# Kernel optimization log

Measured on AMD Instinct MI355X. Metric: run time of the kernel, lower is better.

Reference implementation:

```python
import jax, jax.numpy as jnp
import numpy as np

T, C, NH, NL, NP = 5, 192, 4, 5, 4
DH = C // NH

def leaky(x):
    return jnp.where(x >= 0, x, 0.1 * x)

def conv2d(x, w, b, padding=1, dilation=1):
    out = jax.lax.conv_general_dilated(
        x, w, window_strides=(1, 1),
        padding=[(padding, padding), (padding, padding)],
        rhs_dilation=(dilation, dilation),
        dimension_numbers=('NCHW', 'OIHW', 'NCHW'))
    return out + b[None, :, None, None]

def grid_sample_border(img, gx, gy):
    # align_corners=True, padding_mode='border'; gx/gy normalized [-1,1], shape (B,H,W)
    B, Cc, H, W = img.shape
    x = jnp.clip((gx + 1.0) * 0.5 * (W - 1), 0.0, W - 1)
    y = jnp.clip((gy + 1.0) * 0.5 * (H - 1), 0.0, H - 1)
    x0 = jnp.floor(x); y0 = jnp.floor(y)
    wx = (x - x0).reshape(B, 1, -1); wy = (y - y0).reshape(B, 1, -1)
    flat = img.reshape(B, Cc, H * W)
    def g(yi, xi):
        xi = jnp.clip(xi, 0, W - 1).astype(jnp.int32)
        yi = jnp.clip(yi, 0, H - 1).astype(jnp.int32)
        return jnp.take_along_axis(flat, (yi * W + xi).reshape(B, 1, -1), axis=2)
    out = (g(y0, x0) * (1 - wx) * (1 - wy) + g(y0, x0 + 1) * wx * (1 - wy)
         + g(y0 + 1, x0) * (1 - wx) * wy + g(y0 + 1, x0 + 1) * wx * wy)
    return out.reshape(B, Cc, H, W)

def warp(x, flo):
    B, _, H, W = x.shape
    xx = jnp.arange(W, dtype=jnp.float32)[None, :] * jnp.ones((H, 1), jnp.float32)
    yy = jnp.arange(H, dtype=jnp.float32)[:, None] * jnp.ones((1, W), jnp.float32)
    gx = 2.0 * (xx[None] + flo[:, 0]) / max(W - 1, 1) - 1.0
    gy = 2.0 * (yy[None] + flo[:, 1]) / max(H - 1, 1) - 1.0
    return grid_sample_border(x, gx, gy)

def deform_sample(v_img, loc):
    # v_img (N,D,H,W); loc (N,Q,P,2) in [0,1]; bilinear, zeros padding, align_corners=False
    N, D, H, W = v_img.shape
    Q, P = loc.shape[1], loc.shape[2]
    x = loc[..., 0] * W - 0.5
    y = loc[..., 1] * H - 0.5
    x0 = jnp.floor(x); y0 = jnp.floor(y)
    wx = (x - x0).reshape(N, 1, -1); wy = (y - y0).reshape(N, 1, -1)
    flat = v_img.reshape(N, D, H * W)
    def g(yi, xi):
        valid = ((xi >= 0) & (xi <= W - 1) & (yi >= 0) & (yi <= H - 1)).astype(v_img.dtype)
        xi_c = jnp.clip(xi, 0, W - 1).astype(jnp.int32)
        yi_c = jnp.clip(yi, 0, H - 1).astype(jnp.int32)
        return jnp.take_along_axis(flat, (yi_c * W + xi_c).reshape(N, 1, -1), axis=2) * valid.reshape(N, 1, -1)
    out = (g(y0, x0) * (1 - wx) * (1 - wy) + g(y0, x0 + 1) * wx * (1 - wy)
         + g(y0 + 1, x0) * (1 - wx) * wy + g(y0 + 1, x0 + 1) * wx * wy)
    return out.reshape(N, D, Q, P)

def _forward(frame, srcframe, flow_forward, flow_backward,
             w_qk, b_qk, w_v, b_v, w_vproj, b_vproj, w_off, b_off,
             w_attn, b_attn, w_out, b_out, w_ff, b_ff,
             w_ffn1, b_ffn1, w_ffn2, b_ffn2):
    b, t, c, h, w = frame.shape
    ff01, ff12 = flow_forward[:, 0], flow_forward[:, 1]
    fb32, fb43 = flow_backward[:, 2], flow_backward[:, 3]
    ff02 = ff01 + warp(ff12, ff01)
    fb42 = fb43 + warp(fb32, fb43)
    warp02 = warp(frame[:, 0], ff02)
    warp12 = warp(frame[:, 1], ff12)
    warp32 = warp(frame[:, 3], fb32)
    warp42 = warp(frame[:, 4], fb42)
    qk_in = jnp.concatenate([warp02, warp12, frame[:, 2], warp32, warp42,
                             flow_forward.reshape(b, -1, h, w),
                             flow_backward.reshape(b, -1, h, w)], axis=1)
    queries = leaky(conv2d(qk_in, w_qk, b_qk)).reshape(b, t, c, h, w)
    value = leaky(conv2d(frame.reshape(b, t * c, h, w), w_v, b_v)).reshape(b, t, c, h, w)

    Lq = t * h * w
    q_tok = queries.transpose(0, 1, 3, 4, 2).reshape(b, Lq, c)
    v_tok = value.transpose(0, 1, 3, 4, 2).reshape(b, Lq, c)
    v_proj = (v_tok @ w_vproj.T + b_vproj).reshape(b, t, h * w, NH, DH)

    offs = (q_tok @ w_off.T + b_off).reshape(b, Lq, NH, NL, NP, 2)
    aw = (q_tok @ w_attn.T + b_attn).reshape(b, Lq, NH, NL * NP)
    aw = jax.nn.softmax(aw, axis=-1).reshape(b, Lq, NH, NL, NP)

    # reference points (all valid ratios are ones): ((x+0.5)/W, (y+0.5)/H)
    rx = (jnp.arange(w, dtype=frame.dtype) + 0.5) / w
    ry = (jnp.arange(h, dtype=frame.dtype) + 0.5) / h
    ref = jnp.stack(jnp.meshgrid(rx, ry, indexing='xy'), axis=-1).reshape(h * w, 2)
    ref = jnp.tile(ref, (t, 1))  # (Lq, 2)

    norm = jnp.array([w, h], dtype=frame.dtype)
    # flow-guided per-level displacement toward the center frame (level 2)
    zero = jnp.zeros_like(ff12)
    flows = jnp.stack([ff02, ff12, zero, fb32, fb42], axis=1)  # (b,NL,2,h,w)
    flow_norm = (flows / norm[None, None, :, None, None]).transpose(0, 1, 3, 4, 2).reshape(b, NL, h * w, 2)
    flow_norm = jnp.tile(flow_norm.transpose(0, 2, 1, 3), (1, t, 1, 1))  # (b,Lq,NL,2)

    loc = (ref[None, :, None, None, None, :]
           + offs / norm[None, None, None, None, None, :]
           + flow_norm[:, :, None, :, None, :])  # (b,Lq,NH,NL,NP,2)

    acc = jnp.zeros((b * NH, DH, Lq), dtype=frame.dtype)
    for l in range(NL):
        v_l = v_proj[:, l].transpose(0, 2, 3, 1).reshape(b * NH, DH, h, w)
        loc_l = loc[:, :, :, l].transpose(0, 2, 1, 3, 4).reshape(b * NH, Lq, NP, 2)
        samp = deform_sample(v_l, loc_l)  # (b*NH, DH, Lq, NP)
        w_l = aw[:, :, :, l].transpose(0, 2, 1, 3).reshape(b * NH, 1, Lq, NP)
        acc = acc + (samp * w_l).sum(-1)
    attn = acc.reshape(b, NH, DH, Lq).transpose(0, 3, 1, 2).reshape(b, Lq, c)
    attn = attn @ w_out.T + b_out

    out = attn.reshape(b, t, h, w, c).transpose(0, 1, 4, 2, 3).reshape(b * t, c, h, w)
    out = conv2d(out, w_ff, b_ff)
    out = out.reshape(b, t, c, h, w) + frame
    seq_in = jnp.concatenate([out.reshape(b * t, c, h, w), srcframe.reshape(b * t, c, h, w)], axis=1)
    ffn = conv2d(seq_in, w_ffn1, b_ffn1, padding=2, dilation=2)
    ffn = conv2d(leaky(ffn), w_ffn2, b_ffn2)
    out = out.reshape(b * t, c, h, w) + ffn
    return out.reshape(b, t, c, h, w)

def setup_inputs():
    key = jax.random.key(0)
    ks = jax.random.split(key, 16)
    B, H, W = 2, 64, 64
    s = 0.02
    d = {}
    d['frame'] = jax.random.normal(ks[0], (B, T, C, H, W), jnp.float32)
    d['srcframe'] = jax.random.normal(ks[1], (B, T, C, H, W), jnp.float32)
    d['flow_forward'] = jax.random.normal(ks[2], (B, 4, 2, H, W), jnp.float32)
    d['flow_backward'] = jax.random.normal(ks[3], (B, 4, 2, H, W), jnp.float32)
    cin_qk = T * C + 4 * (T - 1)
    d['w_qk'] = jax.random.normal(ks[4], (T * C, cin_qk, 3, 3), jnp.float32) * s
    d['b_qk'] = jnp.zeros((T * C,), jnp.float32)
    d['w_v'] = jax.random.normal(ks[5], (T * C, T * C, 3, 3), jnp.float32) * s
    d['b_v'] = jnp.zeros((T * C,), jnp.float32)
    d['w_vproj'] = jax.random.normal(ks[6], (C, C), jnp.float32) * s
    d['b_vproj'] = jnp.zeros((C,), jnp.float32)
    d['w_off'] = jax.random.normal(ks[7], (NH * NL * NP * 2, C), jnp.float32) * s
    d['b_off'] = jax.random.normal(ks[8], (NH * NL * NP * 2,), jnp.float32)
    d['w_attn'] = jax.random.normal(ks[9], (NH * NL * NP, C), jnp.float32) * s
    d['b_attn'] = jnp.zeros((NH * NL * NP,), jnp.float32)
    d['w_out'] = jax.random.normal(ks[10], (C, C), jnp.float32) * s
    d['b_out'] = jnp.zeros((C,), jnp.float32)
    d['w_ff'] = jax.random.normal(ks[11], (C, C, 3, 3), jnp.float32) * s
    d['b_ff'] = jnp.zeros((C,), jnp.float32)
    d['w_ffn1'] = jax.random.normal(ks[12], (C, 2 * C, 3, 3), jnp.float32) * s
    d['b_ffn1'] = jnp.zeros((C,), jnp.float32)
    d['w_ffn2'] = jax.random.normal(ks[13], (C, C, 3, 3), jnp.float32) * s
    d['b_ffn2'] = jnp.zeros((C,), jnp.float32)
    return d

def reference(frame, srcframe, flow_forward, flow_backward, w_qk, b_qk, w_v, b_v, w_vproj, b_vproj, w_off, b_off, w_attn, b_attn, w_out, b_out, w_ff, b_ff, w_ffn1, b_ffn1, w_ffn2, b_ffn2):
    out = _forward(frame, srcframe, flow_forward, flow_backward, w_qk, b_qk, w_v, b_v, w_vproj, b_vproj, w_off, b_off, w_attn, b_attn, w_out, b_out, w_ff, b_ff, w_ffn1, b_ffn1, w_ffn2, b_ffn2)
    return (out, srcframe)
```

## Files before the change

### kernel.cpp

```cpp
#include <hip/hip_runtime.h>


#define HWPX 4096
#define PPXN 4624
#define LQ   20480

typedef __attribute__((ext_vector_type(8))) short  short8;
typedef __attribute__((ext_vector_type(4))) short  short4v;
typedef __attribute__((ext_vector_type(4))) float  f32x4;
typedef __attribute__((ext_vector_type(4))) float  float4v;

__device__ __forceinline__ unsigned short f2bf(float f) {
    unsigned u = __float_as_uint(f);
    unsigned r = (u + 0x7FFF + ((u >> 16) & 1)) >> 16;
    return (unsigned short)r;
}
__device__ __forceinline__ float bf2f(unsigned short s) {
    return __uint_as_float(((unsigned)s) << 16);
}

__device__ __forceinline__ void gl_lds16(const unsigned short* g, unsigned short* l) {
    __builtin_amdgcn_global_load_lds(
        (const __attribute__((address_space(1))) unsigned int*)g,
        (__attribute__((address_space(3))) unsigned int*)l, 16, 0, 0);
}

__device__ __forceinline__ float bsample(const float* __restrict__ p, float sx, float sy) {
    sx = fminf(fmaxf(sx, 0.f), 63.f);
    sy = fminf(fmaxf(sy, 0.f), 63.f);
    float x0 = floorf(sx), y0 = floorf(sy);
    int ix0 = (int)x0, iy0 = (int)y0;
    int ix1 = ix0 < 63 ? ix0 + 1 : 63;
    int iy1 = iy0 < 63 ? iy0 + 1 : 63;
    float wx = sx - x0, wy = sy - y0;
    float v00 = p[iy0*64+ix0], v01 = p[iy0*64+ix1];
    float v10 = p[iy1*64+ix0], v11 = p[iy1*64+ix1];
    return (v00*(1.f-wx) + v01*wx)*(1.f-wy) + (v10*(1.f-wx) + v11*wx)*wy;
}

__device__ void dev_flow(int i, const float* __restrict__ ff,
                         const float* __restrict__ fb, float* __restrict__ flows) {
    int b = i >> 12, pix = i & 4095;
    int x = pix & 63, y = pix >> 6;
    const float* ff01 = ff + (size_t)(b*4+0)*2*HWPX;
    const float* ff12 = ff + (size_t)(b*4+1)*2*HWPX;
    const float* fb32 = fb + (size_t)(b*4+2)*2*HWPX;
    const float* fb43 = fb + (size_t)(b*4+3)*2*HWPX;
    float* F = flows + (size_t)b*5*2*HWPX;
    float ax = ff01[pix], ay = ff01[HWPX+pix];
    float sx = bsample(ff12,      (float)x+ax, (float)y+ay);
    float sy = bsample(ff12+HWPX, (float)x+ax, (float)y+ay);
    F[0*2*HWPX + pix]        = ax + sx;
    F[0*2*HWPX + HWPX + pix] = ay + sy;
    F[1*2*HWPX + pix]        = ff12[pix];
    F[1*2*HWPX + HWPX + pix] = ff12[HWPX+pix];
    F[2*2*HWPX + pix]        = 0.f;
    F[2*2*HWPX + HWPX + pix] = 0.f;
    F[3*2*HWPX + pix]        = fb32[pix];
    F[3*2*HWPX + HWPX + pix] = fb32[HWPX+pix];
    float bx = fb43[pix], by = fb43[HWPX+pix];
    float tx = bsample(fb32,      (float)x+bx, (float)y+by);
    float ty = bsample(fb32+HWPX, (float)x+bx, (float)y+by);
    F[4*2*HWPX + pix]        = bx + tx;
    F[4*2*HWPX + HWPX + pix] = by + ty;
}

__device__ void dev_wT(const float* __restrict__ w, unsigned short* __restrict__ wT,
                       int CI, int NKB, int cotile, int kblk, int tid) {
    unsigned short* dst = wT + ((size_t)(cotile*NKB + kblk))*18432;
    #pragma unroll
    for (int it = 0; it < 9; ++it) {
        int idx = it*256 + tid;
        int tap = idx >> 8, sub = idx & 255;
        int cg = sub >> 6, co = sub & 63;
        int cog = cotile*64 + co;
        int ci0 = kblk*32 + cg*8;
        short8 v;
        #pragma unroll
        for (int j = 0; j < 8; ++j) {
            int ci = ci0 + j;
            v[j] = (ci < CI) ? (short)f2bf(w[((size_t)cog*CI + ci)*9 + tap]) : (short)0;
        }
        *(short8*)(dst + (size_t)idx*8) = v;
    }
}

__device__ void dev_wg(const float* __restrict__ w1, const float* __restrict__ w2,
                       unsigned short* __restrict__ wg, int co_split, int CO,
                       int cotile, int tid) {
    unsigned short* dst = wg + (size_t)cotile*12288;
    #pragma unroll
    for (int it = 0; it < 6; ++it) {
        int idx = it*256 + tid;
        int kblk = idx >> 8, sub = idx & 255;
        int cg = sub >> 6, co = sub & 63;
        int cog = cotile*64 + co;
        int ci0 = kblk*32 + cg*8;
        short8 v = {};
        if (cog < CO) {
            const float* row = (cog < co_split) ? w1 + (size_t)cog*192
                                                : w2 + (size_t)(cog - co_split)*192;
            #pragma unroll
            for (int j = 0; j < 8; ++j) v[j] = (short)f2bf(row[ci0 + j]);
        }
        *(short8*)(dst + (size_t)idx*8) = v;
    }
}

__device__ void dev_pad(const float* __restrict__ in, unsigned short* __restrict__ outb,
                        int CI, int PITCH, int COFF, int img, int ppx_t, int cq, int tid) {
    int ppx = ppx_t*64 + (tid & 63);
    if (ppx >= PPXN) return;
    int c8 = (cq*4 + (tid >> 6))*8;
    unsigned short* dst = outb + ((size_t)img*PPXN + ppx)*PITCH;
    int py = ppx/68, pxc = ppx - py*68;
    if (py < 2 || py >= 66 || pxc < 2 || pxc >= 66) {
        short8 z = {};
        *(short8*)(dst + c8) = z;
        if (COFF) *(short8*)(dst + COFF + c8) = z;
        return;
    }
    int pix = ((py-2)<<6) + (pxc-2);
    short8 o;
    #pragma unroll
    for (int j = 0; j < 8; ++j)
        o[j] = (short)f2bf(in[((size_t)img*CI + c8 + j)*HWPX + pix]);
    *(short8*)(dst + COFF + c8) = o;
}

__global__ __launch_bounds__(256) void k_wprep(
    const float* __restrict__ flow_f, const float* __restrict__ flow_b,
    float* __restrict__ flows,
    const float* __restrict__ w_qk, unsigned short* __restrict__ wT_qk,
    const float* __restrict__ w_v,  unsigned short* __restrict__ wT_v,
    const float* __restrict__ w_ff, unsigned short* __restrict__ wT_ff,
    const float* __restrict__ w_f1, unsigned short* __restrict__ wT_f1,
    const float* __restrict__ w_f2, unsigned short* __restrict__ wT_f2,
    const float* __restrict__ w_vp, const float* __restrict__ w_off,
    const float* __restrict__ w_at, const float* __restrict__ w_out,
    unsigned short* __restrict__ wg_vp, unsigned short* __restrict__ wg_oa,
    unsigned short* __restrict__ wg_out,
    const float* __restrict__ srcframe, float* __restrict__ out2)
{
    int bid = blockIdx.x, tid = threadIdx.x;
    if (bid < 32) {
        dev_flow(bid*256 + tid, flow_f, flow_b, flows);
    } else if (bid < 497) {
        int p = bid - 32;   dev_wT(w_qk, wT_qk, 976, 31, p/31, p%31, tid);
    } else if (bid < 947) {
        int p = bid - 497;  dev_wT(w_v,  wT_v,  960, 30, p/30, p%30, tid);
    } else if (bid < 965) {
        int p = bid - 947;  dev_wT(w_ff, wT_ff, 192, 6,  p/6,  p%6,  tid);
    } else if (bid < 1001) {
        int p = bid - 965;  dev_wT(w_f1, wT_f1, 384, 12, p/12, p%12, tid);
    } else if (bid < 1019) {
        int p = bid - 1001; dev_wT(w_f2, wT_f2, 192, 6,  p/6,  p%6,  tid);
    } else if (bid < 1029) {
        int g = bid - 1019;
        if (g < 3)      dev_wg(w_vp,  nullptr, wg_vp, 192, 192, g,   tid);
        else if (g < 7) dev_wg(w_off, w_at,    wg_oa, 160, 240, g-3, tid);
        else            dev_wg(w_out, nullptr, wg_out, 192, 192, g-7, tid);
    } else {
        int c = bid - 1029;
        const float4v* s4 = (const float4v*)srcframe;
        float4v* d4 = (float4v*)out2;
        #pragma unroll
        for (int it = 0; it < 8; ++it) {
            int idx = it*245760 + c*256 + tid;
            d4[idx] = s4[idx];
        }
    }
}

__global__ void k_qkin(const unsigned short* __restrict__ Pv,
                       const float* __restrict__ ff, const float* __restrict__ fb,
                       const float* __restrict__ flows,
                       unsigned short* __restrict__ Pqk)
{
    int ppx = blockIdx.x*64 + threadIdx.x;
    if (ppx >= PPXN) return;
    int b = blockIdx.z;
    int c8 = (blockIdx.y*4 + threadIdx.y)*8;
    unsigned short* dst = Pqk + ((size_t)b*PPXN + ppx)*992 + c8;
    int py = ppx/68, pxc = ppx - py*68;
    short8 o = {};
    if (py >= 2 && py < 66 && pxc >= 2 && pxc < 66 && c8 < 976) {
        int y = py-2, x = pxc-2, pix = (y<<6)+x;
        if (c8 >= 960) {
            #pragma unroll
            for (int j = 0; j < 8; ++j) {
                int k = c8 - 960 + j;
                float v = (k < 8) ? ff[((size_t)b*8 + k)*HWPX + pix]
                                  : fb[((size_t)b*8 + k - 8)*HWPX + pix];
                o[j] = (short)f2bf(v);
            }
        } else {
            const unsigned short* Pvb = Pv + (size_t)b*PPXN*960;
            int slot = c8/192;
            if (slot == 2) {
                o = *(const short8*)(Pvb + (size_t)ppx*960 + c8);
            } else {
                const float* F = flows + ((size_t)(b*5 + slot)*2)*HWPX;
                float sx = fminf(fmaxf((float)x + F[pix], 0.f), 63.f);
                float sy = fminf(fmaxf((float)y + F[HWPX + pix], 0.f), 63.f);
                float x0 = floorf(sx), y0 = floorf(sy);
                int ix0 = (int)x0, iy0 = (int)y0;
                int ix1 = ix0 < 63 ? ix0+1 : 63, iy1 = iy0 < 63 ? iy0+1 : 63;
                float wx = sx - x0, wy = sy - y0;
                float w00 = (1.f-wx)*(1.f-wy), w01 = wx*(1.f-wy);
                float w10 = (1.f-wx)*wy,       w11 = wx*wy;
                short8 v00 = *(const short8*)(Pvb + ((size_t)((iy0+2)*68 + ix0+2))*960 + c8);
                short8 v01 = *(const short8*)(Pvb + ((size_t)((iy0+2)*68 + ix1+2))*960 + c8);
                short8 v10 = *(const short8*)(Pvb + ((size_t)((iy1+2)*68 + ix0+2))*960 + c8);
                short8 v11 = *(const short8*)(Pvb + ((size_t)((iy1+2)*68 + ix1+2))*960 + c8);
                #pragma unroll
                for (int j = 0; j < 8; ++j) {
                    float v = bf2f((unsigned short)v00[j])*w00 + bf2f((unsigned short)v01[j])*w01
                            + bf2f((unsigned short)v10[j])*w10 + bf2f((unsigned short)v11[j])*w11;
                    o[j] = (short)f2bf(v);
                }
            }
        }
    }
    *(short8*)dst = o;
}

__global__ void t_pad(const float* __restrict__ in, unsigned short* __restrict__ outb,
                      int CI, int PITCH, int COFF)
{
    int ppx = blockIdx.x*64 + threadIdx.x;
    if (ppx >= PPXN) return;
    int img = blockIdx.z;
    int c8 = (blockIdx.y*4 + threadIdx.y)*8;
    unsigned short* dst = outb + ((size_t)img*PPXN + ppx)*PITCH;
    int py = ppx/68, pxc = ppx - py*68;
    if (py < 2 || py >= 66 || pxc < 2 || pxc >= 66) {
        short8 z = {};
        *(short8*)(dst + c8) = z;
        if (COFF) *(short8*)(dst + COFF + c8) = z;
        return;
    }
    int pix = ((py-2)<<6) + (pxc-2);
    short8 o;
    #pragma unroll
    for (int j = 0; j < 8; ++j)
        o[j] = (short)f2bf(in[((size_t)img*CI + c8 + j)*HWPX + pix]);
    *(short8*)(dst + COFF + c8) = o;
}

template<int ROWS, int DIL, int OUTK, bool LEAKY, int RESK>
__global__ __launch_bounds__(256, 2) void k_conv(
    const unsigned short* __restrict__ P0, const unsigned short* __restrict__ P1,
    int CIP0, int CIP1, int NKB0, int NKB1,
    const unsigned short* __restrict__ wT0, const unsigned short* __restrict__ wT1,
    const float* __restrict__ bias0, const float* __restrict__ bias1,
    const float* __restrict__ resF, const unsigned short* __restrict__ resB, int resPitch,
    float* __restrict__ outF,
    unsigned short* __restrict__ outB0, unsigned short* __restrict__ outB1,
    int outPitch, int outCoff, int njobs)
{
    constexpr int RR     = ROWS*4 + 2*DIL;
    constexpr int XP     = 64 + 2*DIL;
    constexpr int PLANE  = RR*XP*16;
    constexpr int NCH    = RR*XP*4;
    constexpr int NXS    = (NCH + 255)/256;
    constexpr int TILEPX = ROWS*4*64;
    constexpr int SMEM_K = 4*PLANE + 36864;
    constexpr int SMEM_E = (OUTK <= 1) ? TILEPX*72*2 : 0;
    constexpr int SMEMSZ = SMEM_K > SMEM_E ? SMEM_K : SMEM_E;
    __shared__ __align__(16) unsigned char smem[SMEMSZ];
    unsigned char*  s_x = smem;
    unsigned short* s_w = (unsigned short*)(smem + 4*PLANE);

    int tid = threadIdx.x & 255;
    int gx = gridDim.x, gy = gridDim.y, gz = gridDim.z;
    int lin = blockIdx.x + gx*(blockIdx.y + gy*blockIdx.z);
    int tot = gx*gy*gz;
    if ((tot & 7) == 0) { int q = tot >> 3; lin = (lin & 7)*q + (lin >> 3); }
    int cotile = lin % gx; int rem = lin / gx;
    int ytile = rem % gy;  int z = rem / gy;

    int sel = (njobs == 2) ? (z >> 1) : 0;
    int img = (njobs == 2) ? (z & 1)  : z;
    const unsigned short* P  = sel ? P1  : P0;
    const unsigned short* wT = sel ? wT1 : wT0;
    const float* bias        = sel ? bias1 : bias0;
    unsigned short* outB     = sel ? outB1 : outB0;
    int CIP = sel ? CIP1 : CIP0;
    int NKB = sel ? NKB1 : NKB0;

    int y0 = ytile * (ROWS*4);
    const unsigned short* Pi = P + (size_t)img*PPXN*CIP;
    int w = tid >> 6, lane = tid & 63, lm = lane & 15, cig = lane >> 4;

    auto stage_x = [&](int kb) {
        int k0 = kb*32;
        #pragma unroll
        for (int it = 0; it < NXS; ++it) {
            int li = it*256 + tid;
            if (li < NCH) {
                int p = li / (RR*XP), rm = li - p*(RR*XP);
                int r = rm / XP, c = rm - r*XP;
                gl_lds16(Pi + ((size_t)((y0 + 2 - DIL + r)*68 + c + 2 - DIL))*CIP + k0 + p*8,
                         (unsigned short*)(s_x + li*16));
            }
        }
    };
    auto stage_w = [&](int kb) {
        const unsigned short* ws = wT + ((size_t)(cotile*NKB + kb))*18432;
        #pragma unroll
        for (int it = 0; it < 9; ++it)
            gl_lds16(ws + (size_t)(it*256+tid)*8, &s_w[(it*256+tid)*8]);
    };

    stage_x(0); stage_w(0);
    __syncthreads();

    f32x4 acc[4][ROWS*4] = {};
    for (int kb = 0; kb < NKB; ++kb) {
        __builtin_amdgcn_s_setprio(1);
        #pragma unroll
        for (int t = 0; t < 9; ++t) {
            int ky = t/3, kx = t - ky*3;
            short8 A[4];
            #pragma unroll
            for (int mb = 0; mb < 4; ++mb)
                A[mb] = *(const short8*)&s_w[((t*4 + cig)*64 + mb*16 + lm)*8];
            #pragma unroll
            for (int s = 0; s < ROWS; ++s) {
                short8 Bf[4];
                #pragma unroll
                for (int nc = 0; nc < 4; ++nc)
                    Bf[nc] = *(const short8*)&s_x[cig*PLANE +
                               ((w*ROWS + s + ky*DIL)*XP + nc*16 + lm + kx*DIL)*16];
                #pragma unroll
                for (int mb = 0; mb < 4; ++mb)
                    #pragma unroll
                    for (int nc = 0; nc < 4; ++nc)
                        acc[mb][s*4+nc] = __builtin_amdgcn_mfma_f32_16x16x32_bf16(
                            A[mb], Bf[nc], acc[mb][s*4+nc], 0, 0, 0);
            }
        }
        __builtin_amdgcn_s_setprio(0);
        __syncthreads();
        if (kb + 1 < NKB) { stage_x(kb+1); stage_w(kb+1); }
        __syncthreads();
    }

    if (OUTK == 0 || OUTK == 1) {
        unsigned short* epi = (unsigned short*)smem;
        #pragma unroll
        for (int mb = 0; mb < 4; ++mb) {
            int cob = cotile*64 + mb*16 + cig*4;
            int col = mb*16 + cig*4;
            #pragma unroll
            for (int s = 0; s < ROWS; ++s) {
                int lr = w*ROWS + s;
                #pragma unroll
                for (int nc = 0; nc < 4; ++nc) {
                    int x = nc*16 + lm;
                    int px_l = lr*64 + x;
                    int gpx = y0*64 + px_l;
                    short4v sv;
                    #pragma unroll
                    for (int r = 0; r < 4; ++r) {
                        float v = acc[mb][s*4+nc][r] + bias[cob + r];
                        if (LEAKY) v = v >= 0.f ? v : 0.1f*v;
                        if (RESK == 1) v += resF[((size_t)img*192 + cob + r)*HWPX + gpx];
                        sv[r] = (short)f2bf(v);
                    }
                    *(short4v*)&epi[px_l*72 + col] = sv;
                }
            }
        }
        __syncthreads();
        constexpr int NCPY = TILEPX/32;
        int slot = (OUTK == 0) ? (cotile*64)/192 : 0;
        int ccb  = (OUTK == 0) ? (cotile*64)%192 : (cotile*64 + outCoff);
        #pragma unroll
        for (int it2 = 0; it2 < NCPY; ++it2) {
            int li = it2*256 + tid;
            int px_l = li >> 3, sub = li & 7;
            short8 v = *(const short8*)&epi[px_l*72 + sub*8];
            int gpx = y0*64 + px_l;
            if (OUTK == 0) {
                *(short8*)(outB + ((size_t)(img*5 + slot)*HWPX + gpx)*192 + ccb + sub*8) = v;
            } else {
                int ppx = ((gpx>>6)+2)*68 + (gpx&63) + 2;
                *(short8*)(outB0 + ((size_t)img*PPXN + ppx)*outPitch + ccb + sub*8) = v;
            }
        }
    } else {
        #pragma unroll
        for (int mb = 0; mb < 4; ++mb) {
            int cob = cotile*64 + mb*16 + cig*4;
            #pragma unroll
            for (int s = 0; s < ROWS; ++s) {
                int y = y0 + w*ROWS + s;
                #pragma unroll
                for (int nc = 0; nc < 4; ++nc) {
                    int x = nc*16 + lm;
                    int px = (y<<6) + x;
                    int ppx = (y+2)*68 + x + 2;
                    short4v rv;
                    if (RESK == 2)
                        rv = *(const short4v*)(resB + ((size_t)img*PPXN + ppx)*resPitch + cob);
                    #pragma unroll
                    for (int r = 0; r < 4; ++r) {
                        float v = acc[mb][s*4+nc][r] + bias[cob + r];
                        if (LEAKY) v = v >= 0.f ? v : 0.1f*v;
                        if (RESK == 1) v += resF[((size_t)img*192 + cob + r)*HWPX + px];
                        if (RESK == 2) v += bf2f((unsigned short)rv[r]);
                        outF[((size_t)img*192 + cob + r)*HWPX + px] = v;
                    }
                }
            }
        }
    }
}

#define GEMM_CORE(Xi, WG_, cotile_)                                              \
    _Pragma("unroll")                                                            \
    for (int it = 0; it < 6; ++it)                                               \
        gl_lds16(WG_ + (size_t)(cotile_)*12288 + (it*256+tid)*8,                 \
                 &s_w[(it*256+tid)*8]);                                          \
    short8 xr[4];                                                                \
    _Pragma("unroll")                                                            \
    for (int it = 0; it < 4; ++it)                                               \
        xr[it] = *(const short8*)(Xi + (size_t)(px0 + tid)*192 + it*8);          \
    _Pragma("unroll")                                                            \
    for (int it = 0; it < 4; ++it)                                               \
        *(short8*)&s_x[0][it*4096 + tid*16] = xr[it];                            \
    __syncthreads();                                                             \
    int w = tid >> 6, lane = tid & 63, lm = lane & 15, cig = lane >> 4;          \
    f32x4 acc[4][4] = {};                                                        \
    int xb = 0;                                                                  \
    for (int kb = 0; kb < 6; ++kb) {                                             \
        bool pf = (kb < 5);                                                      \
        if (pf) {                                                                \
            int k0 = (kb+1)*32;                                                  \
            _Pragma("unroll")                                                    \
            for (int it = 0; it < 4; ++it)                                       \
                xr[it] = *(const short8*)(Xi + (size_t)(px0 + tid)*192 + k0 + it*8); \
        }                                                                        \
        short8 A[4], Bf[4];                                                      \
        _Pragma("unroll")                                                        \
        for (int nb = 0; nb < 4; ++nb)                                           \
            Bf[nb] = *(const short8*)&s_x[xb][cig*4096 + (w*64 + nb*16 + lm)*16];\
        _Pragma("unroll")                                                        \
        for (int mb = 0; mb < 4; ++mb)                                           \
            A[mb] = *(const short8*)&s_w[((kb*4 + cig)*64 + mb*16 + lm)*8];      \
        _Pragma("unroll")                                                        \
        for (int mb = 0; mb < 4; ++mb)                                           \
            _Pragma("unroll")                                                    \
            for (int nb = 0; nb < 4; ++nb)                                       \
                acc[mb][nb] = __builtin_amdgcn_mfma_f32_16x16x32_bf16(           \
                    A[mb], Bf[nb], acc[mb][nb], 0, 0, 0);                        \
        if (pf) {                                                                \
            _Pragma("unroll")                                                    \
            for (int it = 0; it < 4; ++it)                                       \
                *(short8*)&s_x[xb^1][it*4096 + tid*16] = xr[it];                 \
        }                                                                        \
        __syncthreads();                                                         \
        xb ^= 1;                                                                 \
    }

__global__ __launch_bounds__(256) void k_gemmA(
    const unsigned short* __restrict__ Xv, const unsigned short* __restrict__ WGv,
    const float* __restrict__ bvp, unsigned short* __restrict__ vp,
    const unsigned short* __restrict__ Xq, const unsigned short* __restrict__ WGq,
    const float* __restrict__ boff, const float* __restrict__ batt,
    float* __restrict__ offs, float* __restrict__ aw,
    unsigned short* __restrict__ P_ff, unsigned short* __restrict__ P_mid)
{
    __shared__ unsigned char  s_x[2][4*4096];
    __shared__ unsigned short s_w[12288];
    int tid = threadIdx.x & 255;
    int id = blockIdx.x;
    if (id < 480) {
        int cotile = id % 3, pxt = (id/3) % 16, img = id/48;
        int px0 = pxt*256;
        const unsigned short* Xi = Xv + (size_t)img*HWPX*192;
        GEMM_CORE(Xi, WGv, cotile)
        #pragma unroll
        for (int mb = 0; mb < 4; ++mb) {
            int cob = cotile*64 + mb*16 + cig*4;
            int h = cob/48, d = cob - h*48;
            #pragma unroll
            for (int nb = 0; nb < 4; ++nb) {
                int px = px0 + w*64 + nb*16 + lm;
                short4v s;
                #pragma unroll
                for (int r = 0; r < 4; ++r)
                    s[r] = (short)f2bf(acc[mb][nb][r] + bvp[cob + r]);
                *(short4v*)(vp + (((size_t)img*4 + h)*HWPX + px)*48 + d) = s;
            }
        }
    } else if (id < 1120) {
        int i2 = id - 480;
        int cotile = i2 % 4, pxt = (i2/4) % 16, img = i2/64;
        int px0 = pxt*256;
        const unsigned short* Xi = Xq + (size_t)img*HWPX*192;
        GEMM_CORE(Xi, WGq, cotile)
        int b = img/5, t = img - b*5;
        #pragma unroll
        for (int mb = 0; mb < 4; ++mb) {
            int cob = cotile*64 + mb*16 + cig*4;
            if (cob >= 240) continue;
            #pragma unroll
            for (int nb = 0; nb < 4; ++nb) {
                int px = px0 + w*64 + nb*16 + lm;
                #pragma unroll
                for (int r = 0; r < 4; ++r) {
                    int co = cob + r;
                    float bv = (co < 160) ? boff[co] : batt[co-160];
                    float v = acc[mb][nb][r] + bv;
                    if (co < 160) offs[((size_t)b*160 + co)*LQ + t*HWPX + px] = v;
                    else          aw[((size_t)b*80 + co-160)*LQ + t*HWPX + px] = v;
                }
            }
        }
    } else {
        int u = (id - 1120)*256 + tid;
        int c8i = u % 24; int r1 = u / 24;
        int b = r1 % 528; int r2 = r1 / 528;
        int img = r2 % 10; int buf = r2 / 10;
        int ppx;
        if (b < 136) ppx = b;
        else if (b < 272) ppx = 4488 + (b - 136);
        else { int b2 = b - 272; int row = 2 + (b2 >> 2); int cs = b2 & 3;
               ppx = row*68 + ((cs < 2) ? cs : cs + 64); }
        unsigned short* bp2 = buf ? P_mid : P_ff;
        short8 z = {};
        *(short8*)(bp2 + ((size_t)img*PPXN + ppx)*192 + c8i*8) = z;
    }
}

__global__ __launch_bounds__(256) void k_tailB(
    const unsigned short* __restrict__ X, const unsigned short* __restrict__ WG,
    const float* __restrict__ b1, unsigned short* __restrict__ P_ff,
    const float* __restrict__ srcframe, unsigned short* __restrict__ P_ffn1)
{
    __shared__ unsigned char  s_x[2][4*4096];
    __shared__ unsigned short s_w[12288];
    int tid = threadIdx.x & 255;
    int id = blockIdx.x;
    if (id < 480) {
        int cotile = id % 3, pxt = (id/3) % 16, img = id/48;
        int px0 = pxt*256;
        const unsigned short* Xi = X + (size_t)img*HWPX*192;
        GEMM_CORE(Xi, WG, cotile)
        #pragma unroll
        for (int mb = 0; mb < 4; ++mb) {
            int cob = cotile*64 + mb*16 + cig*4;
            #pragma unroll
            for (int nb = 0; nb < 4; ++nb) {
                int px = px0 + w*64 + nb*16 + lm;
                int ppx = ((px>>6)+2)*68 + (px&63) + 2;
                short4v s;
                #pragma unroll
                for (int r = 0; r < 4; ++r)
                    s[r] = (short)f2bf(acc[mb][nb][r] + b1[cob + r]);
                *(short4v*)(P_ff + ((size_t)img*PPXN + ppx)*192 + cob) = s;
            }
        }
    } else {
        int p = id - 480;
        int img = p / 438, rem = p - img*438;
        int ppx_t = rem % 73, cq = rem / 73;
        dev_pad(srcframe, P_ffn1, 192, 384, 192, img, ppx_t, cq, tid);
    }
}

__device__ __forceinline__ void addtap24(float* acc, const unsigned short* __restrict__ src, float w) {
    const short8* s8 = (const short8*)src;
    #pragma unroll
    for (int u = 0; u < 3; ++u) {
        short8 v = s8[u];
        #pragma unroll
        for (int j = 0; j < 8; ++j)
            acc[u*8+j] += w * bf2f((unsigned short)v[j]);
    }
}

__global__ __launch_bounds__(256) void k_sample(
    const unsigned short* __restrict__ vp, const float* __restrict__ offs,
    const float* __restrict__ aw, const float* __restrict__ flows,
    unsigned short* __restrict__ accout)
{
    int blk = blockIdx.x;
    int b = blk / 640, sub = blk - b*640;
    int tid = threadIdx.x;
    int lq = sub*32 + (tid >> 3);
    int h = (tid >> 1) & 3, q = tid & 1;
    int pix = lq & 4095;
    int x = pix & 63, y = pix >> 6;
    const float* offp = offs + ((size_t)b*160 + h*40)*LQ + lq;
    const float* awp  = aw   + ((size_t)b*80  + h*20)*LQ + lq;
    float e[20];
    float m = -1e30f;
    #pragma unroll
    for (int j = 0; j < 20; ++j) { e[j] = awp[(size_t)j*LQ]; m = fmaxf(m, e[j]); }
    float ssum = 0.f;
    #pragma unroll
    for (int j = 0; j < 20; ++j) { e[j] = __expf(e[j]-m); ssum += e[j]; }
    float inv = 1.f/ssum;

    float acc[24];
    #pragma unroll
    for (int d = 0; d < 24; ++d) acc[d] = 0.f;

    for (int l = 0; l < 5; ++l) {
        float fx = flows[((size_t)(b*5+l)*2+0)*HWPX + pix];
        float fy = flows[((size_t)(b*5+l)*2+1)*HWPX + pix];
        const unsigned short* vpl = vp + (((size_t)(b*5+l)*4 + h)*HWPX)*48 + q*24;
        #pragma unroll
        for (int p = 0; p < 4; ++p) {
            int o = l*4 + p;
            float ox = offp[(size_t)(2*o)*LQ];
            float oy = offp[(size_t)(2*o+1)*LQ];
            float wv = e[o]*inv;
            float sx = (float)x + ox + fx;
            float sy = (float)y + oy + fy;
            float x0f = floorf(sx), y0f = floorf(sy);
            float wx = sx - x0f, wy = sy - y0f;
            int ix0 = (int)x0f, iy0 = (int)y0f;
            float w00 = wv*(1.f-wx)*(1.f-wy), w01 = wv*wx*(1.f-wy);
            float w10 = wv*(1.f-wx)*wy,       w11 = wv*wx*wy;
            bool vx0 = (ix0 >= 0)  && (ix0 <= 63);
            bool vx1 = (ix0 >= -1) && (ix0 <= 62);
            bool vy0 = (iy0 >= 0)  && (iy0 <= 63);
            bool vy1 = (iy0 >= -1) && (iy0 <= 62);
            if (vy0 && vx0) addtap24(acc, vpl + (size_t)(iy0*64 + ix0)*48,       w00);
            if (vy0 && vx1) addtap24(acc, vpl + (size_t)(iy0*64 + ix0 + 1)*48,   w01);
            if (vy1 && vx0) addtap24(acc, vpl + (size_t)((iy0+1)*64 + ix0)*48,   w10);
            if (vy1 && vx1) addtap24(acc, vpl + (size_t)((iy0+1)*64 + ix0+1)*48, w11);
        }
    }
    unsigned short* dst = accout + ((size_t)b*LQ + lq)*192 + h*48 + q*24;
    #pragma unroll
    for (int u = 0; u < 3; ++u) {
        short8 s;
        #pragma unroll
        for (int j = 0; j < 8; ++j) s[j] = (short)f2bf(acc[u*8+j]);
        *(short8*)(dst + u*8) = s;
    }
}


extern "C" void kernel_launch(void* const* d_in, const int* in_sizes, int n_in,
                              void* d_out, int out_size, void* d_ws, size_t ws_size,
                              hipStream_t stream) {
    (void)in_sizes; (void)n_in; (void)out_size; (void)ws_size;
    const float* frame    = (const float*)d_in[0];
    const float* srcframe = (const float*)d_in[1];
    const float* flow_f   = (const float*)d_in[2];
    const float* flow_b   = (const float*)d_in[3];
    const float* w_qk  = (const float*)d_in[4];  const float* b_qk  = (const float*)d_in[5];
    const float* w_v   = (const float*)d_in[6];  const float* b_v   = (const float*)d_in[7];
    const float* w_vp  = (const float*)d_in[8];  const float* b_vp  = (const float*)d_in[9];
    const float* w_off = (const float*)d_in[10]; const float* b_off = (const float*)d_in[11];
    const float* w_at  = (const float*)d_in[12]; const float* b_at  = (const float*)d_in[13];
    const float* w_out = (const float*)d_in[14]; const float* b_out = (const float*)d_in[15];
    const float* w_ff  = (const float*)d_in[16]; const float* b_ff  = (const float*)d_in[17];
    const float* w_f1  = (const float*)d_in[18]; const float* b_f1  = (const float*)d_in[19];
    const float* w_f2  = (const float*)d_in[20]; const float* b_f2  = (const float*)d_in[21];
    float* out = (float*)d_out;
    char* W = (char*)d_ws;

    float*          flows  = (float*)(W + 0);
    unsigned short* wT_qk  = (unsigned short*)(W + 327680);
    unsigned short* wT_v   = (unsigned short*)(W + 17469440);
    unsigned short* P_qk   = (unsigned short*)(W + 34058240);
    unsigned short* P_ff   = P_qk;
    unsigned short* P_v    = (unsigned short*)(W + 52406272);
    unsigned short* P_mid  = P_v;
    unsigned short* Q_tok  = (unsigned short*)(W + 70162432);
    unsigned short* acc_tok= Q_tok;
    unsigned short* V_tok  = (unsigned short*)(W + 85891072);
    unsigned short* P_ffn1 = V_tok;
    unsigned short* vp     = (unsigned short*)(W + 101619712);
    float*          offs   = (float*)(W + 121403392);
    float*          aw     = (float*)(W + 147617792);
    unsigned short* wT_ff  = (unsigned short*)(W + 160724992);
    unsigned short* wT_f1  = (unsigned short*)(W + 161388544);
    unsigned short* wT_f2  = (unsigned short*)(W + 162715648);
    unsigned short* wg_vp  = (unsigned short*)(W + 163379200);
    unsigned short* wg_oa  = (unsigned short*)(W + 163452928);
    unsigned short* wg_out = (unsigned short*)(W + 163551232);

    dim3 bp(64, 4);

    k_wprep<<<1989, 256, 0, stream>>>(
        flow_f, flow_b, flows,
        w_qk, wT_qk, w_v, wT_v, w_ff, wT_ff, w_f1, wT_f1, w_f2, wT_f2,
        w_vp, w_off, w_at, w_out, wg_vp, wg_oa, wg_out,
        srcframe, out + (size_t)2*5*192*HWPX);
    t_pad<<<dim3(73,30,2), bp, 0, stream>>>(frame, P_v, 960, 960, 0);
    k_qkin<<<dim3(73,31,2), bp, 0, stream>>>(P_v, flow_f, flow_b, flows, P_qk);
    k_conv<2,1,0,true,0><<<dim3(15,8,4), 256, 0, stream>>>(
        P_qk, P_v, 992, 960, 31, 30, wT_qk, wT_v, b_qk, b_v,
        nullptr, nullptr, 0, nullptr, Q_tok, V_tok, 0, 0, 2);
    k_gemmA<<<2110, 256, 0, stream>>>(
        V_tok, wg_vp, b_vp, vp, Q_tok, wg_oa, b_off, b_at, offs, aw, P_ff, P_mid);
    k_sample<<<1280, 256, 0, stream>>>(vp, offs, aw, flows, acc_tok);
    k_tailB<<<4860, 256, 0, stream>>>(acc_tok, wg_out, b_out, P_ff,
                                      srcframe, P_ffn1);
    k_conv<1,1,1,false,1><<<dim3(3,16,10), 256, 0, stream>>>(
        P_ff, nullptr, 192, 0, 6, 0, wT_ff, nullptr, b_ff, nullptr,
        frame, nullptr, 0, nullptr, P_ffn1, nullptr, 384, 0, 1);
    k_conv<1,2,1,true,0><<<dim3(3,16,10), 256, 0, stream>>>(
        P_ffn1, nullptr, 384, 0, 12, 0, wT_f1, nullptr, b_f1, nullptr,
        nullptr, nullptr, 0, nullptr, P_mid, nullptr, 192, 0, 1);
    k_conv<1,1,2,false,2><<<dim3(3,16,10), 256, 0, stream>>>(
        P_mid, nullptr, 192, 0, 6, 0, wT_f2, nullptr, b_f2, nullptr,
        nullptr, P_ffn1, 384, out, nullptr, nullptr, 0, 0, 1);
}
```

Baseline: 807.8 us.

## Split deformable sampling points across thread pairs and fold padding into prep kernel

k_sample now splits the 20 sampling points of each query/head across two threads, each handling 10 points. The two partial accumulators are combined with a shuffle-xor reduction and only one thread writes, so twice as many blocks run with fewer serial gathers per thread. Separately, the frame padding/bf16 conversion kernel is merged into the k_wprep launch as extra blocks, removing one kernel launch. The cost is extra shuffles and more blocks in the sampling kernel. Merging also ties the pad work to the prep kernel's block scheduling.

```diff
diff --git a/kernel.cpp b/kernel.cpp
--- a/kernel.cpp
+++ b/kernel.cpp
@@ -140,7 +140,8 @@
     const float* __restrict__ w_at, const float* __restrict__ w_out,
     unsigned short* __restrict__ wg_vp, unsigned short* __restrict__ wg_oa,
     unsigned short* __restrict__ wg_out,
-    const float* __restrict__ srcframe, float* __restrict__ out2)
+    const float* __restrict__ srcframe, float* __restrict__ out2,
+    const float* __restrict__ frame, unsigned short* __restrict__ P_v)
 {
     int bid = blockIdx.x, tid = threadIdx.x;
     if (bid < 32) {
@@ -160,7 +161,7 @@
         if (g < 3)      dev_wg(w_vp,  nullptr, wg_vp, 192, 192, g,   tid);
         else if (g < 7) dev_wg(w_off, w_at,    wg_oa, 160, 240, g-3, tid);
         else            dev_wg(w_out, nullptr, wg_out, 192, 192, g-7, tid);
-    } else {
+    } else if (bid < 1989) {
         int c = bid - 1029;
         const float4v* s4 = (const float4v*)srcframe;
         float4v* d4 = (float4v*)out2;
@@ -169,6 +170,11 @@
             int idx = it*245760 + c*256 + tid;
             d4[idx] = s4[idx];
         }
+    } else {
+        int p = bid - 1989;
+        int img = p / 2190, rem = p - img*2190;
+        int ppx_t = rem % 73, cq = rem / 73;
+        dev_pad(frame, P_v, 960, 960, 0, img, ppx_t, cq, tid);
     }
 }
 
@@ -223,29 +229,6 @@
         }
     }
     *(short8*)dst = o;
-}
-
-__global__ void t_pad(const float* __restrict__ in, unsigned short* __restrict__ outb,
-                      int CI, int PITCH, int COFF)
-{
-    int ppx = blockIdx.x*64 + threadIdx.x;
-    if (ppx >= PPXN) return;
-    int img = blockIdx.z;
-    int c8 = (blockIdx.y*4 + threadIdx.y)*8;
-    unsigned short* dst = outb + ((size_t)img*PPXN + ppx)*PITCH;
-    int py = ppx/68, pxc = ppx - py*68;
-    if (py < 2 || py >= 66 || pxc < 2 || pxc >= 66) {
-        short8 z = {};
-        *(short8*)(dst + c8) = z;
-        if (COFF) *(short8*)(dst + COFF + c8) = z;
-        return;
-    }
-    int pix = ((py-2)<<6) + (pxc-2);
-    short8 o;
-    #pragma unroll
-    for (int j = 0; j < 8; ++j)
-        o[j] = (short)f2bf(in[((size_t)img*CI + c8 + j)*HWPX + pix]);
-    *(short8*)(dst + COFF + c8) = o;
 }
 
 template<int ROWS, int DIL, int OUTK, bool LEAKY, int RESK>
@@ -589,10 +572,12 @@
     unsigned short* __restrict__ accout)
 {
     int blk = blockIdx.x;
-    int b = blk / 640, sub = blk - b*640;
+    int b = blk / 1280, sub = blk - b*1280;
     int tid = threadIdx.x;
-    int lq = sub*32 + (tid >> 3);
-    int h = (tid >> 1) & 3, q = tid & 1;
+    int lq = sub*16 + (tid >> 4);
+    int h  = (tid >> 2) & 3;
+    int qt = (tid >> 1) & 1;
+    int qc = tid & 1;
     int pix = lq & 4095;
     int x = pix & 63, y = pix >> 6;
     const float* offp = offs + ((size_t)b*160 + h*40)*LQ + lq;
@@ -610,40 +595,46 @@
     #pragma unroll
     for (int d = 0; d < 24; ++d) acc[d] = 0.f;
 
-    for (int l = 0; l < 5; ++l) {
+    int o0 = qt*10;
+    #pragma unroll
+    for (int oi = 0; oi < 10; ++oi) {
+        int o = o0 + oi;
+        int l = o >> 2, p = o & 3;
+        (void)p;
         float fx = flows[((size_t)(b*5+l)*2+0)*HWPX + pix];
         float fy = flows[((size_t)(b*5+l)*2+1)*HWPX + pix];
-        const unsigned short* vpl = vp + (((size_t)(b*5+l)*4 + h)*HWPX)*48 + q*24;
-        #pragma unroll
-        for (int p = 0; p < 4; ++p) {
-            int o = l*4 + p;
-            float ox = offp[(size_t)(2*o)*LQ];
-            float oy = offp[(size_t)(2*o+1)*LQ];
-            float wv = e[o]*inv;
-            float sx = (float)x + ox + fx;
-            float sy = (float)y + oy + fy;
-            float x0f = floorf(sx), y0f = floorf(sy);
-            float wx = sx - x0f, wy = sy - y0f;
-            int ix0 = (int)x0f, iy0 = (int)y0f;
-            float w00 = wv*(1.f-wx)*(1.f-wy), w01 = wv*wx*(1.f-wy);
-            float w10 = wv*(1.f-wx)*wy,       w11 = wv*wx*wy;
-            bool vx0 = (ix0 >= 0)  && (ix0 <= 63);
-            bool vx1 = (ix0 >= -1) && (ix0 <= 62);
-            bool vy0 = (iy0 >= 0)  && (iy0 <= 63);
-            bool vy1 = (iy0 >= -1) && (iy0 <= 62);
-            if (vy0 && vx0) addtap24(acc, vpl + (size_t)(iy0*64 + ix0)*48,       w00);
-            if (vy0 && vx1) addtap24(acc, vpl + (size_t)(iy0*64 + ix0 + 1)*48,   w01);
-            if (vy1 && vx0) addtap24(acc, vpl + (size_t)((iy0+1)*64 + ix0)*48,   w10);
-            if (vy1 && vx1) addtap24(acc, vpl + (size_t)((iy0+1)*64 + ix0+1)*48, w11);
-        }
-    }
-    unsigned short* dst = accout + ((size_t)b*LQ + lq)*192 + h*48 + q*24;
-    #pragma unroll
-    for (int u = 0; u < 3; ++u) {
-        short8 s;
-        #pragma unroll
-        for (int j = 0; j < 8; ++j) s[j] = (short)f2bf(acc[u*8+j]);
-        *(short8*)(dst + u*8) = s;
+        const unsigned short* vpl = vp + (((size_t)(b*5+l)*4 + h)*HWPX)*48 + qc*24;
+        float ox = offp[(size_t)(2*o)*LQ];
+        float oy = offp[(size_t)(2*o+1)*LQ];
+        float wv = e[o]*inv;
+        float sx = (float)x + ox + fx;
+        float sy = (float)y + oy + fy;
+        float x0f = floorf(sx), y0f = floorf(sy);
+        float wx = sx - x0f, wy = sy - y0f;
+        int ix0 = (int)x0f, iy0 = (int)y0f;
+        float w00 = wv*(1.f-wx)*(1.f-wy), w01 = wv*wx*(1.f-wy);
+        float w10 = wv*(1.f-wx)*wy,       w11 = wv*wx*wy;
+        bool vx0 = (ix0 >= 0)  && (ix0 <= 63);
+        bool vx1 = (ix0 >= -1) && (ix0 <= 62);
+        bool vy0 = (iy0 >= 0)  && (iy0 <= 63);
+        bool vy1 = (iy0 >= -1) && (iy0 <= 62);
+        if (vy0 && vx0) addtap24(acc, vpl + (size_t)(iy0*64 + ix0)*48,       w00);
+        if (vy0 && vx1) addtap24(acc, vpl + (size_t)(iy0*64 + ix0 + 1)*48,   w01);
+        if (vy1 && vx0) addtap24(acc, vpl + (size_t)((iy0+1)*64 + ix0)*48,   w10);
+        if (vy1 && vx1) addtap24(acc, vpl + (size_t)((iy0+1)*64 + ix0+1)*48, w11);
+    }
+    #pragma unroll
+    for (int d = 0; d < 24; ++d)
+        acc[d] += __shfl_xor(acc[d], 2);
+    if (qt == 0) {
+        unsigned short* dst = accout + ((size_t)b*LQ + lq)*192 + h*48 + qc*24;
+        #pragma unroll
+        for (int u = 0; u < 3; ++u) {
+            short8 s;
+            #pragma unroll
+            for (int j = 0; j < 8; ++j) s[j] = (short)f2bf(acc[u*8+j]);
+            *(short8*)(dst + u*8) = s;
+        }
     }
 }
 
@@ -691,19 +682,18 @@
 
     dim3 bp(64, 4);
 
-    k_wprep<<<1989, 256, 0, stream>>>(
+    k_wprep<<<6369, 256, 0, stream>>>(
         flow_f, flow_b, flows,
         w_qk, wT_qk, w_v, wT_v, w_ff, wT_ff, w_f1, wT_f1, w_f2, wT_f2,
         w_vp, w_off, w_at, w_out, wg_vp, wg_oa, wg_out,
-        srcframe, out + (size_t)2*5*192*HWPX);
-    t_pad<<<dim3(73,30,2), bp, 0, stream>>>(frame, P_v, 960, 960, 0);
+        srcframe, out + (size_t)2*5*192*HWPX, frame, P_v);
     k_qkin<<<dim3(73,31,2), bp, 0, stream>>>(P_v, flow_f, flow_b, flows, P_qk);
     k_conv<2,1,0,true,0><<<dim3(15,8,4), 256, 0, stream>>>(
         P_qk, P_v, 992, 960, 31, 30, wT_qk, wT_v, b_qk, b_v,
         nullptr, nullptr, 0, nullptr, Q_tok, V_tok, 0, 0, 2);
     k_gemmA<<<2110, 256, 0, stream>>>(
         V_tok, wg_vp, b_vp, vp, Q_tok, wg_oa, b_off, b_at, offs, aw, P_ff, P_mid);
-    k_sample<<<1280, 256, 0, stream>>>(vp, offs, aw, flows, acc_tok);
+    k_sample<<<2560, 256, 0, stream>>>(vp, offs, aw, flows, acc_tok);
     k_tailB<<<4860, 256, 0, stream>>>(acc_tok, wg_out, b_out, P_ff,
                                       srcframe, P_ffn1);
     k_conv<1,1,1,false,1><<<dim3(3,16,10), 256, 0, stream>>>(
```

After: 811.0 us. About the same (+0.4%).
